# Performance work log

Measured on AMD Instinct MI355X. Metric: run time of the kernel, lower is better.

The kernel has to match this reference:

```python
import jax, jax.numpy as jnp
import numpy as np

B, S, D, H, L = 2, 1024, 1024, 16, 4
HD = D // H          # head_dim = 64
M = 2730             # swiglu hidden = int(4*D*2/3)
V = 32000


def setup_inputs() -> dict:
    key = jax.random.key(0)
    ks = jax.random.split(key, 10)
    w = lambda k, shape: jax.random.normal(k, shape, jnp.float32) * 0.02
    return {
        "tokens": jax.random.randint(ks[0], (B, S), 0, V, dtype=jnp.int32),
        "embed": w(ks[1], (V, D)),
        "Wqkv": w(ks[2], (L, D, 3 * D)), "bqkv": jnp.zeros((L, 3 * D), jnp.float32),
        "Wout": w(ks[3], (L, D, D)), "bout": jnp.zeros((L, D), jnp.float32),
        "ln1": jnp.ones((L, D), jnp.float32), "ln2": jnp.ones((L, D), jnp.float32),
        "Wg": w(ks[4], (L, D, M)), "bg": jnp.zeros((L, M), jnp.float32),
        "Wu": w(ks[5], (L, D, M)), "bu": jnp.zeros((L, M), jnp.float32),
        "Wd": w(ks[6], (L, M, D)), "bd": jnp.zeros((L, D), jnp.float32),
        "lnf": jnp.ones((D,), jnp.float32),
        "Whead": w(ks[7], (D, V)), "bhead": jnp.zeros((V,), jnp.float32),
    }


def rmsnorm(x, scale, eps=1e-6):
    return x * jax.lax.rsqrt(jnp.mean(x * x, axis=-1, keepdims=True) + eps) * scale


def rope_cache(seq_len, dim, base=10000.0):
    rot_dim = dim // 2 * 2
    inv_freq = 1.0 / base ** (jnp.arange(0, rot_dim, 2) / rot_dim)
    freqs = jnp.arange(seq_len)[:, None] * inv_freq[None, :]  # (S, HD//2)
    return jnp.cos(freqs), jnp.sin(freqs)


def rotate(x, cos, sin):
    # x: (B,H,S,HD); cos/sin: (1,1,S,HD//2); interleaved even/odd rotation
    e, o = x[..., 0::2], x[..., 1::2]
    re = e * cos - o * sin
    ro = e * sin + o * cos
    return jnp.stack([re, ro], axis=-1).reshape(x.shape)


def forward(tokens, embed, Wqkv, bqkv, Wout, bout, ln1, ln2,
            Wg, bg, Wu, bu, Wd, bd, lnf, Whead, bhead):
    x = embed[tokens]                                   # (B,S,D)
    cos, sin = rope_cache(S, HD)
    cos, sin = cos[None, None], sin[None, None]
    mask = jnp.tril(jnp.ones((S, S), bool))
    scale = HD ** -0.5
    for l in range(L):
        # attention (pre-norm)
        h = rmsnorm(x, ln1[l])
        qkv = (h @ Wqkv[l] + bqkv[l]).reshape(B, S, 3, H, HD)
        qkv = jnp.transpose(qkv, (2, 0, 3, 1, 4))       # (3,B,H,S,HD)
        q, k, v = qkv[0], qkv[1], qkv[2]
        q, k = rotate(q, cos, sin), rotate(k, cos, sin)
        aw = jnp.einsum('bhqd,bhkd->bhqk', q, k) * scale
        aw = jax.nn.softmax(jnp.where(mask, aw, -1e9), axis=-1)
        o = jnp.einsum('bhqk,bhkd->bhqd', aw, v)
        o = jnp.transpose(o, (0, 2, 1, 3)).reshape(B, S, D)
        x = x + (o @ Wout[l] + bout[l])
        # SwiGLU MLP (pre-norm)
        h = rmsnorm(x, ln2[l])
        h = jax.nn.silu(h @ Wg[l] + bg[l]) * (h @ Wu[l] + bu[l])
        x = x + (h @ Wd[l] + bd[l])
    x = rmsnorm(x, lnf)
    return x[:, -1, :] @ Whead + bhead                  # (B, V)


def reference(tokens, embed, Wqkv, bqkv, Wout, bout, ln1, ln2,
              Wg, bg, Wu, bu, Wd, bd, lnf, Whead, bhead):
    return forward(tokens, embed, Wqkv, bqkv, Wout, bout, ln1, ln2,
                   Wg, bg, Wu, bu, Wd, bd, lnf, Whead, bhead)
```

## Files before the change

### kernel.cpp

```cpp
#include <hip/hip_runtime.h>

#define B_   2
#define S_   1024
#define D_   1024
#define H_   16
#define HD_  64
#define L_   4
#define MFF  2730
#define MPAD 2816
#define V_   32000

typedef __attribute__((ext_vector_type(8))) short   short8;
typedef __attribute__((ext_vector_type(4))) float   floatx4;

__device__ __forceinline__ unsigned short f2b(float f) {
  unsigned u = __float_as_uint(f);
  u += 0x7fffu + ((u >> 16) & 1u);
  return (unsigned short)(u >> 16);
}
__device__ __forceinline__ float b2f(unsigned short s) {
  return __uint_as_float(((unsigned)s) << 16);
}

__device__ __forceinline__ void gload16(const unsigned short* g, unsigned short* l) {
  __builtin_amdgcn_global_load_lds(
      (const __attribute__((address_space(1))) unsigned int*)(unsigned long long)g,
      (__attribute__((address_space(3))) unsigned int*)(unsigned int)(unsigned long long)l,
      16, 0, 0);
}

__global__ __launch_bounds__(256) void embed_kernel(const int* __restrict__ tokens,
                                                    const float* __restrict__ embed,
                                                    float* __restrict__ x) {
  int row = blockIdx.x;
  int tok = tokens[row];
  int c = threadIdx.x * 4;
  float4 v = *(const float4*)&embed[(size_t)tok * D_ + c];
  *(float4*)&x[(size_t)row * D_ + c] = v;
}

__global__ __launch_bounds__(256) void rmsnorm_bf(const float* __restrict__ x,
                                                  const float* __restrict__ w,
                                                  unsigned short* __restrict__ out) {
  int row = blockIdx.x, t = threadIdx.x;
  float4 xv = *(const float4*)&x[(size_t)row * D_ + t * 4];
  float ss = xv.x * xv.x + xv.y * xv.y + xv.z * xv.z + xv.w * xv.w;
  #pragma unroll
  for (int off = 1; off < 64; off <<= 1) ss += __shfl_xor(ss, off, 64);
  __shared__ float sred[4];
  if ((t & 63) == 0) sred[t >> 6] = ss;
  __syncthreads();
  ss = sred[0] + sred[1] + sred[2] + sred[3];
  float rr = rsqrtf(ss * (1.f / (float)D_) + 1e-6f);
  float4 wv = *(const float4*)&w[t * 4];
  size_t o = (size_t)row * D_ + t * 4;
  out[o + 0] = f2b(xv.x * rr * wv.x);
  out[o + 1] = f2b(xv.y * rr * wv.y);
  out[o + 2] = f2b(xv.z * rr * wv.z);
  out[o + 3] = f2b(xv.w * rr * wv.w);
}

__global__ __launch_bounds__(256) void rmsnorm_final(const float* __restrict__ x,
                                                     const float* __restrict__ w,
                                                     float* __restrict__ out) {
  int b = blockIdx.x, t = threadIdx.x;
  const float* xr = x + ((size_t)b * S_ + (S_ - 1)) * D_;
  float4 xv = *(const float4*)&xr[t * 4];
  float ss = xv.x * xv.x + xv.y * xv.y + xv.z * xv.z + xv.w * xv.w;
  #pragma unroll
  for (int off = 1; off < 64; off <<= 1) ss += __shfl_xor(ss, off, 64);
  __shared__ float sred[4];
  if ((t & 63) == 0) sred[t >> 6] = ss;
  __syncthreads();
  ss = sred[0] + sred[1] + sred[2] + sred[3];
  float rr = rsqrtf(ss * (1.f / (float)D_) + 1e-6f);
  float4 wv = *(const float4*)&w[t * 4];
  size_t o = (size_t)b * D_ + t * 4;
  out[o + 0] = xv.x * rr * wv.x;
  out[o + 1] = xv.y * rr * wv.y;
  out[o + 2] = xv.z * rr * wv.z;
  out[o + 3] = xv.w * rr * wv.w;
}

__global__ __launch_bounds__(256) void transpose_conv(const float* __restrict__ W,
                                                      unsigned short* __restrict__ Wt,
                                                      int K, int N, int Kpad, int Npad) {
  __shared__ float tile[64][65];
  const int tx = threadIdx.x & 15, ty = threadIdx.x >> 4;
  const int k0 = blockIdx.y * 64, n0 = blockIdx.x * 64;
  #pragma unroll
  for (int i = 0; i < 4; i++) {
    int kk = k0 + ty + i * 16;
    int nn = n0 + tx * 4;
    float4 v = {0.f, 0.f, 0.f, 0.f};
    if (kk < K) {
      if (nn + 3 < N) v = *(const float4*)&W[(size_t)kk * N + nn];
      else {
        if (nn + 0 < N) v.x = W[(size_t)kk * N + nn + 0];
        if (nn + 1 < N) v.y = W[(size_t)kk * N + nn + 1];
        if (nn + 2 < N) v.z = W[(size_t)kk * N + nn + 2];
      }
    }
    tile[ty + i * 16][tx * 4 + 0] = v.x;
    tile[ty + i * 16][tx * 4 + 1] = v.y;
    tile[ty + i * 16][tx * 4 + 2] = v.z;
    tile[ty + i * 16][tx * 4 + 3] = v.w;
  }
  __syncthreads();
  #pragma unroll
  for (int i = 0; i < 4; i++) {
    int nn = n0 + ty + i * 16;
    int kk = k0 + tx * 4;
    if (nn < Npad && kk < Kpad) {
      ushort4 o;
      o.x = f2b(tile[tx * 4 + 0][ty + i * 16]);
      o.y = f2b(tile[tx * 4 + 1][ty + i * 16]);
      o.z = f2b(tile[tx * 4 + 2][ty + i * 16]);
      o.w = f2b(tile[tx * 4 + 3][ty + i * 16]);
      *(ushort4*)&Wt[(size_t)nn * Kpad + kk] = o;
    }
  }
}

template <int EPI, int MTILE>
__global__ __launch_bounds__(256) void gemm_bt(const unsigned short* __restrict__ A,
                                               const unsigned short* __restrict__ B,
                                               const float* __restrict__ bias,
                                               const float* __restrict__ res,
                                               void* __restrict__ Cout,
                                               int N, int K, int lda, int ldb, int ldc,
                                               int Nlog) {
  constexpr int MW = MTILE / 32;
  __shared__ unsigned short As[MTILE * 32];
  __shared__ unsigned short Bs[128 * 32];
  const int tid = threadIdx.x;
  const int lane = tid & 63, wave = tid >> 6;
  const int m0 = blockIdx.y * MTILE, n0 = blockIdx.x * 128;
  const int rS = tid >> 2;
  const int kS = (tid & 3) * 8;
  const int fr = lane & 15;
  const int kq = (lane >> 4) * 8;
  const int wm = (wave & 1) * (MTILE / 2), wn = (wave >> 1) * 64;

  floatx4 zv = {0.f, 0.f, 0.f, 0.f};
  floatx4 acc[MW][4];
  #pragma unroll
  for (int mi = 0; mi < MW; mi++)
    #pragma unroll
    for (int ni = 0; ni < 4; ni++) acc[mi][ni] = zv;

  for (int k0 = 0; k0 < K; k0 += 32) {
    __syncthreads();
    #pragma unroll
    for (int i = 0; i < MTILE / 64; i++)
      gload16(A + (size_t)(m0 + i * 64 + rS) * lda + k0 + kS, &As[i * 2048 + wave * 512]);
    #pragma unroll
    for (int i = 0; i < 2; i++)
      gload16(B + (size_t)(n0 + i * 64 + rS) * ldb + k0 + kS, &Bs[i * 2048 + wave * 512]);
    __syncthreads();
    short8 af[MW], bfv[4];
    #pragma unroll
    for (int mi = 0; mi < MW; mi++) af[mi] = *(const short8*)&As[(wm + mi * 16 + fr) * 32 + kq];
    #pragma unroll
    for (int ni = 0; ni < 4; ni++) bfv[ni] = *(const short8*)&Bs[(wn + ni * 16 + fr) * 32 + kq];
    #pragma unroll
    for (int mi = 0; mi < MW; mi++)
      #pragma unroll
      for (int ni = 0; ni < 4; ni++)
        acc[mi][ni] = __builtin_amdgcn_mfma_f32_16x16x32_bf16(af[mi], bfv[ni], acc[mi][ni], 0, 0, 0);
  }

  const int cr = (lane >> 4) * 4;
  const int cc = lane & 15;
  #pragma unroll
  for (int mi = 0; mi < MW; mi++) {
    #pragma unroll
    for (int ni = 0; ni < 4; ni++) {
      int col = n0 + wn + ni * 16 + cc;
      float bv = (col < Nlog) ? bias[col] : 0.f;
      #pragma unroll
      for (int r = 0; r < 4; r++) {
        int row = m0 + wm + mi * 16 + cr + r;
        float val = acc[mi][ni][r] + bv;
        if constexpr (EPI == 1) val += res[(size_t)row * ldc + col];
        if constexpr (EPI == 2)
          ((unsigned short*)Cout)[(size_t)row * ldc + col] = f2b(val);
        else
          ((float*)Cout)[(size_t)row * ldc + col] = val;
      }
    }
  }
}

__global__ __launch_bounds__(256) void rope_table(float* __restrict__ cs, float* __restrict__ sn) {
  int i = blockIdx.x * 256 + threadIdx.x;
  int s = i >> 5, f = i & 31;
  double inv = pow(10000.0, -(double)(2 * f) / 64.0);
  double ang = (double)s * inv;
  cs[i] = (float)cos(ang);
  sn[i] = (float)sin(ang);
}

__global__ __launch_bounds__(256) void rope_apply(const unsigned short* __restrict__ qkv,
                                                  const float* __restrict__ cs,
                                                  const float* __restrict__ sn,
                                                  unsigned short* __restrict__ q,
                                                  unsigned short* __restrict__ k,
                                                  unsigned short* __restrict__ v) {
  int i = blockIdx.x * 256 + threadIdx.x;
  int pr = i & 31;
  int h  = (i >> 5) & 15;
  int s  = (i >> 9) & 1023;
  int b  = i >> 19;
  size_t base = ((size_t)(b * S_ + s)) * (3 * D_) + h * HD_ + pr * 2;
  unsigned qp = *(const unsigned*)&qkv[base];
  unsigned kp = *(const unsigned*)&qkv[base + D_];
  unsigned vp = *(const unsigned*)&qkv[base + 2 * D_];
  float qe = b2f((unsigned short)qp), qo = b2f((unsigned short)(qp >> 16));
  float ke = b2f((unsigned short)kp), ko = b2f((unsigned short)(kp >> 16));
  float c = cs[s * 32 + pr], sv = sn[s * 32 + pr];
  size_t ob = ((size_t)(b * H_ + h)) * (S_ * HD_) + (size_t)s * HD_ + pr * 2;
  unsigned qw = (unsigned)f2b(qe * c - qo * sv) | ((unsigned)f2b(qe * sv + qo * c) << 16);
  unsigned kw = (unsigned)f2b(ke * c - ko * sv) | ((unsigned)f2b(ke * sv + ko * c) << 16);
  *(unsigned*)&q[ob] = qw;
  *(unsigned*)&k[ob] = kw;
  *(unsigned*)&v[ob] = vp;
}

__global__ __launch_bounds__(256) void vtrans(const unsigned short* __restrict__ v,
                                              unsigned short* __restrict__ vT) {
  __shared__ unsigned short t[64][72];
  const int st = blockIdx.x, bh = blockIdx.y;
  const int row = threadIdx.x >> 2, c = (threadIdx.x & 3) * 16;
  const unsigned short* vb = v + (size_t)bh * (S_ * HD_);
  unsigned short* vo = vT + (size_t)bh * (HD_ * S_);
  *(uint4*)&t[row][c]     = *(const uint4*)&vb[(size_t)(st * 64 + row) * HD_ + c];
  *(uint4*)&t[row][c + 8] = *(const uint4*)&vb[(size_t)(st * 64 + row) * HD_ + c + 8];
  __syncthreads();
  unsigned short buf[16];
  #pragma unroll
  for (int j = 0; j < 16; j++) buf[j] = t[c + j][row];
  *(uint4*)&vo[(size_t)row * S_ + st * 64 + c]     = *(uint4*)&buf[0];
  *(uint4*)&vo[(size_t)row * S_ + st * 64 + c + 8] = *(uint4*)&buf[8];
}

__global__ __launch_bounds__(256) void attn_mfma(const unsigned short* __restrict__ qg,
                                                 const unsigned short* __restrict__ kg,
                                                 const unsigned short* __restrict__ vTg,
                                                 unsigned short* __restrict__ o) {
  __shared__ unsigned short ks[64 * 72];
  __shared__ unsigned short vs[64 * 72];
  __shared__ unsigned short ps[64 * 72];
  const int qt = (S_ / 64 - 1) - blockIdx.x;
  const int bh = blockIdx.y;
  const int b = bh >> 4, h = bh & 15;
  const unsigned short* qb = qg + (size_t)bh * (S_ * HD_);
  const unsigned short* kb = kg + (size_t)bh * (S_ * HD_);
  const unsigned short* vb = vTg + (size_t)bh * (HD_ * S_);
  const int tid = threadIdx.x, lane = tid & 63, wave = tid >> 6;
  const int fr = lane & 15;
  const int kq8 = (lane >> 4) * 8;
  const int srow = tid >> 2;
  const int sc = (tid & 3) * 16;

  short8 qf[2];
  {
    const int qrow = qt * 64 + wave * 16 + fr;
    qf[0] = *(const short8*)&qb[(size_t)qrow * HD_ + kq8];
    qf[1] = *(const short8*)&qb[(size_t)qrow * HD_ + 32 + kq8];
  }
  floatx4 zv = {0.f, 0.f, 0.f, 0.f};
  float m_run[4], l_run[4];
  floatx4 oacc[4];
  #pragma unroll
  for (int r = 0; r < 4; r++) { m_run[r] = -1e30f; l_run[r] = 0.f; }
  #pragma unroll
  for (int di = 0; di < 4; di++) oacc[di] = zv;

  const int rbase = wave * 16 + (lane >> 4) * 4;

  for (int kt = 0; kt <= qt; kt++) {
    if (kt) __syncthreads();
    {
      const unsigned short* kr = &kb[(size_t)(kt * 64 + srow) * HD_ + sc];
      *(uint4*)&ks[srow * 72 + sc]     = *(const uint4*)kr;
      *(uint4*)&ks[srow * 72 + sc + 8] = *(const uint4*)(kr + 8);
      const unsigned short* vr = &vb[(size_t)srow * S_ + kt * 64 + sc];
      *(uint4*)&vs[srow * 72 + sc]     = *(const uint4*)vr;
      *(uint4*)&vs[srow * 72 + sc + 8] = *(const uint4*)(vr + 8);
    }
    __syncthreads();
    floatx4 s4[4];
    #pragma unroll
    for (int ni = 0; ni < 4; ni++) {
      short8 kf0 = *(const short8*)&ks[(ni * 16 + fr) * 72 + kq8];
      short8 kf1 = *(const short8*)&ks[(ni * 16 + fr) * 72 + 32 + kq8];
      floatx4 a = __builtin_amdgcn_mfma_f32_16x16x32_bf16(qf[0], kf0, zv, 0, 0, 0);
      s4[ni] = __builtin_amdgcn_mfma_f32_16x16x32_bf16(qf[1], kf1, a, 0, 0, 0);
    }
    const bool diag = (kt == qt);
    #pragma unroll
    for (int r = 0; r < 4; r++) {
      float sr[4];
      #pragma unroll
      for (int ni = 0; ni < 4; ni++) {
        float sv = s4[ni][r] * 0.125f;
        if (diag && (ni * 16 + fr > rbase + r)) sv = -1e9f;
        sr[ni] = sv;
      }
      float mx = fmaxf(fmaxf(sr[0], sr[1]), fmaxf(sr[2], sr[3]));
      #pragma unroll
      for (int off = 1; off < 16; off <<= 1) mx = fmaxf(mx, __shfl_xor(mx, off, 64));
      float mn = fmaxf(m_run[r], mx);
      float alpha = __expf(m_run[r] - mn);
      float rs = 0.f;
      #pragma unroll
      for (int ni = 0; ni < 4; ni++) {
        float pv = __expf(sr[ni] - mn);
        rs += pv;
        ps[(rbase + r) * 72 + ni * 16 + fr] = f2b(pv);
      }
      #pragma unroll
      for (int off = 1; off < 16; off <<= 1) rs += __shfl_xor(rs, off, 64);
      l_run[r] = l_run[r] * alpha + rs;
      m_run[r] = mn;
      #pragma unroll
      for (int di = 0; di < 4; di++) oacc[di][r] *= alpha;
    }
    #pragma unroll
    for (int kp = 0; kp < 2; kp++) {
      short8 pa = *(const short8*)&ps[(wave * 16 + fr) * 72 + kp * 32 + kq8];
      #pragma unroll
      for (int di = 0; di < 4; di++) {
        short8 vf = *(const short8*)&vs[(di * 16 + fr) * 72 + kp * 32 + kq8];
        oacc[di] = __builtin_amdgcn_mfma_f32_16x16x32_bf16(pa, vf, oacc[di], 0, 0, 0);
      }
    }
  }
  float inv[4];
  #pragma unroll
  for (int r = 0; r < 4; r++) inv[r] = 1.f / l_run[r];
  #pragma unroll
  for (int di = 0; di < 4; di++) {
    #pragma unroll
    for (int r = 0; r < 4; r++) {
      int srow_g = qt * 64 + rbase + r;
      o[((size_t)(b * S_ + srow_g)) * D_ + h * HD_ + di * 16 + fr] = f2b(oacc[di][r] * inv[r]);
    }
  }
}

__global__ __launch_bounds__(256) void concat_bias(const float* __restrict__ bg_,
                                                   const float* __restrict__ bu_,
                                                   float* __restrict__ bgu) {
  int n = blockIdx.x * 256 + threadIdx.x;
  float v = 0.f;
  if (n < MPAD) { if (n < MFF) v = bg_[n]; }
  else { int m = n - MPAD; if (m < MFF) v = bu_[m]; }
  bgu[n] = v;
}

__global__ __launch_bounds__(256) void swiglu_kernel(const unsigned short* __restrict__ gu,
                                                     unsigned short* __restrict__ act) {
  int n = blockIdx.x * 256 + threadIdx.x;
  int row = blockIdx.y;
  float a = 0.f;
  if (n < MFF) {
    float gv = b2f(gu[(size_t)row * (2 * MPAD) + n]);
    float uv = b2f(gu[(size_t)row * (2 * MPAD) + MPAD + n]);
    a = gv / (1.f + __expf(-gv)) * uv;
  }
  act[(size_t)row * MPAD + n] = f2b(a);
}

__global__ __launch_bounds__(256) void head_kernel(const float* __restrict__ hf,
                                                   const float* __restrict__ Wh,
                                                   const float* __restrict__ bh_,
                                                   float* __restrict__ out) {
  __shared__ float hs[2 * D_];
  __shared__ float r0[256][4], r1[256][4];
  const int t = threadIdx.x;
  {
    float4* hs4 = (float4*)hs;
    const float4* hf4 = (const float4*)hf;
    hs4[t] = hf4[t];
    hs4[t + 256] = hf4[t + 256];
  }
  __syncthreads();
  const int cg  = t & 15;
  const int ksl = t >> 4;
  const int col = blockIdx.x * 64 + cg * 4;
  const float* wp  = Wh + (size_t)(ksl * 64) * V_ + col;
  const float* h0p = &hs[ksl * 64];
  const float* h1p = &hs[D_ + ksl * 64];
  float a0x = 0.f, a0y = 0.f, a0z = 0.f, a0w = 0.f;
  float a1x = 0.f, a1y = 0.f, a1z = 0.f, a1w = 0.f;
  #pragma unroll 8
  for (int k = 0; k < 64; k++) {
    float4 w = *(const float4*)(wp + (size_t)k * V_);
    float h0 = h0p[k], h1 = h1p[k];
    a0x = fmaf(h0, w.x, a0x); a0y = fmaf(h0, w.y, a0y);
    a0z = fmaf(h0, w.z, a0z); a0w = fmaf(h0, w.w, a0w);
    a1x = fmaf(h1, w.x, a1x); a1y = fmaf(h1, w.y, a1y);
    a1z = fmaf(h1, w.z, a1z); a1w = fmaf(h1, w.w, a1w);
  }
  r0[t][0] = a0x; r0[t][1] = a0y; r0[t][2] = a0z; r0[t][3] = a0w;
  r1[t][0] = a1x; r1[t][1] = a1y; r1[t][2] = a1z; r1[t][3] = a1w;
  __syncthreads();
  if (t < 16) {
    float s0[4] = {0.f, 0.f, 0.f, 0.f}, s1[4] = {0.f, 0.f, 0.f, 0.f};
    #pragma unroll
    for (int s = 0; s < 16; s++) {
      #pragma unroll
      for (int j = 0; j < 4; j++) {
        s0[j] += r0[s * 16 + t][j];
        s1[j] += r1[s * 16 + t][j];
      }
    }
    int c = blockIdx.x * 64 + t * 4;
    float4 bv = *(const float4*)&bh_[c];
    float4 o0 = {s0[0] + bv.x, s0[1] + bv.y, s0[2] + bv.z, s0[3] + bv.w};
    float4 o1 = {s1[0] + bv.x, s1[1] + bv.y, s1[2] + bv.z, s1[3] + bv.w};
    *(float4*)&out[c]      = o0;
    *(float4*)&out[V_ + c] = o1;
  }
}

extern "C" void kernel_launch(void* const* d_in, const int* in_sizes, int n_in,
                              void* d_out, int out_size, void* d_ws, size_t ws_size,
                              hipStream_t stream) {
  const int*   tokens = (const int*)d_in[0];
  const float* embed  = (const float*)d_in[1];
  const float* Wqkv   = (const float*)d_in[2];
  const float* bqkv   = (const float*)d_in[3];
  const float* Wout   = (const float*)d_in[4];
  const float* bout   = (const float*)d_in[5];
  const float* ln1    = (const float*)d_in[6];
  const float* ln2    = (const float*)d_in[7];
  const float* Wg     = (const float*)d_in[8];
  const float* bg     = (const float*)d_in[9];
  const float* Wu     = (const float*)d_in[10];
  const float* bu     = (const float*)d_in[11];
  const float* Wd     = (const float*)d_in[12];
  const float* bd     = (const float*)d_in[13];
  const float* lnf    = (const float*)d_in[14];
  const float* Whead  = (const float*)d_in[15];
  const float* bhead  = (const float*)d_in[16];
  float* out = (float*)d_out;

  char* base = (char*)d_ws;
  size_t off = 0;
  auto alloc = [&](size_t bytes) -> char* {
    char* r = base + off;
    off += (bytes + 255) & ~(size_t)255;
    return r;
  };
  const size_t NROW = (size_t)B_ * S_;
  unsigned short* WqkvT = (unsigned short*)alloc((size_t)L_ * 3072 * 1024 * 2);
  unsigned short* WoutT = (unsigned short*)alloc((size_t)L_ * 1024 * 1024 * 2);
  unsigned short* WguT  = (unsigned short*)alloc((size_t)L_ * 2 * MPAD * 1024 * 2);
  unsigned short* WdT   = (unsigned short*)alloc((size_t)L_ * 1024 * MPAD * 2);
  float*          x     = (float*)alloc(NROW * D_ * 4);
  unsigned short* h     = (unsigned short*)alloc(NROW * D_ * 2);
  unsigned short* qkv   = (unsigned short*)alloc(NROW * 3072 * 2);
  unsigned short* qb    = (unsigned short*)alloc(NROW * HD_ * H_ * 2);
  unsigned short* kb    = (unsigned short*)alloc(NROW * HD_ * H_ * 2);
  unsigned short* vb    = (unsigned short*)alloc(NROW * HD_ * H_ * 2);
  unsigned short* vT    = (unsigned short*)alloc(NROW * HD_ * H_ * 2);
  unsigned short* gu    = (unsigned short*)alloc(NROW * 2 * MPAD * 2);
  float*          bgu   = (float*)alloc(2 * MPAD * 4);
  float*          csT   = (float*)alloc((size_t)S_ * 32 * 4);
  float*          snT   = (float*)alloc((size_t)S_ * 32 * 4);
  float*          hfin  = (float*)alloc((size_t)B_ * D_ * 4);
  unsigned short* act   = qkv;
  unsigned short* aout  = vb;

  for (int l = 0; l < L_; l++) {
    transpose_conv<<<dim3(3072 / 64, 1024 / 64), 256, 0, stream>>>(
        Wqkv + (size_t)l * 1024 * 3072, WqkvT + (size_t)l * 3072 * 1024, 1024, 3072, 1024, 3072);
    transpose_conv<<<dim3(1024 / 64, 1024 / 64), 256, 0, stream>>>(
        Wout + (size_t)l * 1024 * 1024, WoutT + (size_t)l * 1024 * 1024, 1024, 1024, 1024, 1024);
    transpose_conv<<<dim3(MPAD / 64, 1024 / 64), 256, 0, stream>>>(
        Wg + (size_t)l * 1024 * MFF, WguT + (size_t)l * 2 * MPAD * 1024, 1024, MFF, 1024, MPAD);
    transpose_conv<<<dim3(MPAD / 64, 1024 / 64), 256, 0, stream>>>(
        Wu + (size_t)l * 1024 * MFF, WguT + (size_t)l * 2 * MPAD * 1024 + (size_t)MPAD * 1024,
        1024, MFF, 1024, MPAD);
    transpose_conv<<<dim3(1024 / 64, MPAD / 64), 256, 0, stream>>>(
        Wd + (size_t)l * MFF * 1024, WdT + (size_t)l * 1024 * MPAD, MFF, 1024, MPAD, 1024);
  }
  rope_table<<<dim3(S_ * 32 / 256), 256, 0, stream>>>(csT, snT);
  embed_kernel<<<dim3(NROW), 256, 0, stream>>>(tokens, embed, x);

  for (int l = 0; l < L_; l++) {
    rmsnorm_bf<<<dim3(NROW), 256, 0, stream>>>(x, ln1 + (size_t)l * D_, h);
    gemm_bt<2, 128><<<dim3(3072 / 128, NROW / 128), 256, 0, stream>>>(
        h, WqkvT + (size_t)l * 3072 * 1024, bqkv + (size_t)l * 3072, nullptr, qkv,
        3072, 1024, 1024, 1024, 3072, 3072);
    rope_apply<<<dim3((B_ * S_ * H_ * 32) / 256), 256, 0, stream>>>(qkv, csT, snT, qb, kb, vb);
    vtrans<<<dim3(S_ / 64, B_ * H_), 256, 0, stream>>>(vb, vT);
    attn_mfma<<<dim3(S_ / 64, B_ * H_), 256, 0, stream>>>(qb, kb, vT, aout);
    gemm_bt<1, 64><<<dim3(1024 / 128, NROW / 64), 256, 0, stream>>>(
        aout, WoutT + (size_t)l * 1024 * 1024, bout + (size_t)l * D_, x, x,
        1024, 1024, 1024, 1024, 1024, 1024);
    rmsnorm_bf<<<dim3(NROW), 256, 0, stream>>>(x, ln2 + (size_t)l * D_, h);
    concat_bias<<<dim3(2 * MPAD / 256), 256, 0, stream>>>(
        bg + (size_t)l * MFF, bu + (size_t)l * MFF, bgu);
    gemm_bt<2, 128><<<dim3(2 * MPAD / 128, NROW / 128), 256, 0, stream>>>(
        h, WguT + (size_t)l * 2 * MPAD * 1024, bgu, nullptr, gu,
        2 * MPAD, 1024, 1024, 1024, 2 * MPAD, 2 * MPAD);
    swiglu_kernel<<<dim3(MPAD / 256, NROW), 256, 0, stream>>>(gu, act);
    gemm_bt<1, 64><<<dim3(1024 / 128, NROW / 64), 256, 0, stream>>>(
        act, WdT + (size_t)l * 1024 * MPAD, bd + (size_t)l * D_, x, x,
        1024, MPAD, MPAD, MPAD, 1024, 1024);
  }

  rmsnorm_final<<<dim3(B_), 256, 0, stream>>>(x, lnf, hfin);
  head_kernel<<<dim3(V_ / 64), 256, 0, stream>>>(hfin, Whead, bhead, out);
}
```

Before: 1.369 ms.

## Double-buffer GEMM LDS tiles with async prefetch and vmcnt waits

The bf16 GEMM main loop now uses two LDS buffers for the A and B tiles. It issues global-to-LDS loads for the next k-tile before computing on the current one, and waits with explicit s_waitcnt vmcnt counts before a raw s_barrier. The aim is to hide global load latency behind MFMA work instead of stalling twice per iteration with __syncthreads. This doubles LDS use and relies on hand-counted outstanding loads, which are only correct when the load count is 3 or 4 per stage.

```diff
diff --git a/kernel.cpp b/kernel.cpp
--- a/kernel.cpp
+++ b/kernel.cpp
@@ -27,6 +27,12 @@
       (const __attribute__((address_space(1))) unsigned int*)(unsigned long long)g,
       (__attribute__((address_space(3))) unsigned int*)(unsigned int)(unsigned long long)l,
       16, 0, 0);
+}
+
+__device__ __forceinline__ void wgbar() {
+  asm volatile("" ::: "memory");
+  __builtin_amdgcn_s_barrier();
+  asm volatile("" ::: "memory");
 }
 
 __global__ __launch_bounds__(256) void embed_kernel(const int* __restrict__ tokens,
@@ -131,8 +137,9 @@
                                                int N, int K, int lda, int ldb, int ldc,
                                                int Nlog) {
   constexpr int MW = MTILE / 32;
-  __shared__ unsigned short As[MTILE * 32];
-  __shared__ unsigned short Bs[128 * 32];
+  constexpr int LOADS = MTILE / 64 + 2;
+  __shared__ unsigned short As[2][MTILE * 32];
+  __shared__ unsigned short Bs[2][128 * 32];
   const int tid = threadIdx.x;
   const int lane = tid & 63, wave = tid >> 6;
   const int m0 = blockIdx.y * MTILE, n0 = blockIdx.x * 128;
@@ -142,6 +149,9 @@
   const int kq = (lane >> 4) * 8;
   const int wm = (wave & 1) * (MTILE / 2), wn = (wave >> 1) * 64;
 
+  const unsigned short* Ab = A + (size_t)(m0 + rS) * lda + kS;
+  const unsigned short* Bb = B + (size_t)(n0 + rS) * ldb + kS;
+
   floatx4 zv = {0.f, 0.f, 0.f, 0.f};
   floatx4 acc[MW][4];
   #pragma unroll
@@ -149,25 +159,41 @@
     #pragma unroll
     for (int ni = 0; ni < 4; ni++) acc[mi][ni] = zv;
 
-  for (int k0 = 0; k0 < K; k0 += 32) {
-    __syncthreads();
+  auto stage = [&](int buf, int k0) {
     #pragma unroll
     for (int i = 0; i < MTILE / 64; i++)
-      gload16(A + (size_t)(m0 + i * 64 + rS) * lda + k0 + kS, &As[i * 2048 + wave * 512]);
+      gload16(Ab + (size_t)(i * 64) * lda + k0, &As[buf][i * 2048 + wave * 512]);
     #pragma unroll
     for (int i = 0; i < 2; i++)
-      gload16(B + (size_t)(n0 + i * 64 + rS) * ldb + k0 + kS, &Bs[i * 2048 + wave * 512]);
-    __syncthreads();
+      gload16(Bb + (size_t)(i * 64) * ldb + k0, &Bs[buf][i * 2048 + wave * 512]);
+  };
+
+  const int nk = K / 32;
+  stage(0, 0);
+  int cur = 0;
+  for (int kt = 0; kt < nk; kt++) {
+    if (kt + 1 < nk) {
+      stage(cur ^ 1, (kt + 1) * 32);
+      if constexpr (LOADS == 4)
+        asm volatile("s_waitcnt vmcnt(4)" ::: "memory");
+      else
+        asm volatile("s_waitcnt vmcnt(3)" ::: "memory");
+    } else {
+      asm volatile("s_waitcnt vmcnt(0)" ::: "memory");
+    }
+    wgbar();
     short8 af[MW], bfv[4];
     #pragma unroll
-    for (int mi = 0; mi < MW; mi++) af[mi] = *(const short8*)&As[(wm + mi * 16 + fr) * 32 + kq];
-    #pragma unroll
-    for (int ni = 0; ni < 4; ni++) bfv[ni] = *(const short8*)&Bs[(wn + ni * 16 + fr) * 32 + kq];
+    for (int mi = 0; mi < MW; mi++) af[mi] = *(const short8*)&As[cur][(wm + mi * 16 + fr) * 32 + kq];
+    #pragma unroll
+    for (int ni = 0; ni < 4; ni++) bfv[ni] = *(const short8*)&Bs[cur][(wn + ni * 16 + fr) * 32 + kq];
     #pragma unroll
     for (int mi = 0; mi < MW; mi++)
       #pragma unroll
       for (int ni = 0; ni < 4; ni++)
         acc[mi][ni] = __builtin_amdgcn_mfma_f32_16x16x32_bf16(af[mi], bfv[ni], acc[mi][ni], 0, 0, 0);
+    wgbar();
+    cur ^= 1;
   }
 
   const int cr = (lane >> 4) * 4;
```

Result: faster. 1.246 ms (-8.9%).
